# Kernel tuning notes

Measured on AMD Instinct MI355X. Metric: run time of the kernel, lower is better.

Reference implementation:

```python
import jax, jax.numpy as jnp
import numpy as np

B, S, E, H = 1, 4096, 768, 12
DH = E // H  # 64


def setup_inputs() -> dict:
    key = jax.random.key(0)
    ks = jax.random.split(key, 4)
    x = jax.random.normal(ks[0], (B, S, E), dtype=jnp.float32)
    mask = jnp.tril(jnp.ones((S, S), dtype=bool))  # causal mask, broadcast over B,H
    w_qkv = jax.random.normal(ks[1], (3 * E, E), dtype=jnp.float32) * 0.02
    b_qkv = jnp.zeros((3 * E,), dtype=jnp.float32)
    w_out = jax.random.normal(ks[2], (E, E), dtype=jnp.float32) * 0.02
    b_out = jnp.zeros((E,), dtype=jnp.float32)
    return {"x": x, "mask": mask, "w_qkv": w_qkv, "b_qkv": b_qkv,
            "w_out": w_out, "b_out": b_out}


def reference(x, mask, w_qkv, b_qkv, w_out, b_out):
    b, s, e = x.shape
    # qkv projection: torch Linear is x @ W^T + b
    qkv = x @ w_qkv.T + b_qkv                      # [B,S,3E]
    q, k, v = jnp.split(qkv, 3, axis=-1)           # each [B,S,E]
    def heads(t):
        return t.reshape(b, s, H, DH).transpose(0, 2, 1, 3)  # [B,H,S,Dh]
    q, k, v = heads(q), heads(k), heads(v)
    # NOTE: original module does NOT scale by 1/sqrt(head_dim)
    scores = jnp.einsum('bhqd,bhkd->bhqk', q, k)   # [B,H,S,S]
    scores = jnp.where(mask, scores, -jnp.inf)     # masked_fill(mask==0, -inf)
    probs = jax.nn.softmax(scores, axis=-1)        # dropout=0 (eval)
    attn = jnp.einsum('bhqk,bhkd->bhqd', probs, v) # [B,H,S,Dh]
    attn = attn.transpose(0, 2, 1, 3).reshape(b, s, e)
    return attn @ w_out.T + b_out
```

## Files before the change

kernel.cpp:

```cpp
#include <hip/hip_runtime.h>
#include <hip/hip_bf16.h>

#define S_LEN 4096
#define EMB   768
#define NH    12
#define DH    64
#define NCHUNK 4
#define CKL2   10

#define LOG2E 1.44269504088896f

#define NEG_BIG (-1e30f)

#define EXP2F(x) __builtin_amdgcn_exp2f(x)

using bf16x8 = __attribute__((ext_vector_type(8))) short;
using bf16x4 = __attribute__((ext_vector_type(4))) short;
using f32x4  = __attribute__((ext_vector_type(4))) float;

__device__ __forceinline__ short f2bf(float f) {
    __hip_bfloat16 h = __float2bfloat16(f);
    short s; __builtin_memcpy(&s, &h, 2); return s;
}
__device__ __forceinline__ float bf2f(short s) {
    __hip_bfloat16 h; __builtin_memcpy(&h, &s, 2);
    return __bfloat162float(h);
}

__device__ __forceinline__ unsigned cvt_pk_bf16(float a, float b) {
    unsigned r;
    asm("v_cvt_pk_bf16_f32 %0, %1, %2" : "=v"(r) : "v"(a), "v"(b));
    return r;
}

__device__ __forceinline__ void gld_lds16(const void* g, void* l) {
    __builtin_amdgcn_global_load_lds(
        (const __attribute__((address_space(1))) unsigned int*)g,
        (__attribute__((address_space(3))) unsigned int*)l, 16, 0, 0);
}

__device__ __forceinline__ void cvt8(const float* s, short* d, int i) {
    const float4 a = ((const float4*)s)[i * 2];
    const float4 b = ((const float4*)s)[i * 2 + 1];
    bf16x8 o;
    o[0] = f2bf(a.x); o[1] = f2bf(a.y); o[2] = f2bf(a.z); o[3] = f2bf(a.w);
    o[4] = f2bf(b.x); o[5] = f2bf(b.y); o[6] = f2bf(b.z); o[7] = f2bf(b.w);
    ((bf16x8*)d)[i] = o;
}

__global__ __launch_bounds__(256) void cvt_bf16(
    const float* __restrict__ s, short* __restrict__ d, int n8)
{
    const int i = blockIdx.x * 256 + threadIdx.x;
    if (i < n8) cvt8(s, d, i);
}

__global__ __launch_bounds__(256) void cvt3_bf16(
    const float* __restrict__ x,  short* __restrict__ xb,  int n8x,
    const float* __restrict__ wq, short* __restrict__ wqb, int n8q,
    const float* __restrict__ wo, short* __restrict__ wob, int n8o)
{
    int i = blockIdx.x * 256 + threadIdx.x;
    if (i < n8x) { cvt8(x, xb, i); return; }
    i -= n8x;
    if (i < n8q) { cvt8(wq, wqb, i); return; }
    i -= n8q;
    if (i < n8o) cvt8(wo, wob, i);
}

__global__ __launch_bounds__(256) void qkv_gemm(
    const short* __restrict__ Xb, const short* __restrict__ Wb,
    const float* __restrict__ Bias,
    short* __restrict__ Qw, short* __restrict__ Kw, short* __restrict__ Vt)
{
    __shared__ __align__(16) short SMEM[2 * 128 * 64];
    short* As = SMEM;
    short* Bs = SMEM + 128 * 64;

    const int flat = blockIdx.x;
    const int swz = (flat & 7) * 72 + (flat >> 3);
    const int m0 = (swz / 18) * 128;
    const int n0 = (swz % 18) * 128;
    const int t = threadIdx.x;
    const int lane = t & 63, wave = t >> 6;
    const int quad = lane >> 4, l16 = lane & 15;
    const int wm = (wave >> 1) * 64, wn = (wave & 1) * 64;
    const int srow = lane >> 3, scol = (lane & 7) * 8;

    f32x4 acc[4][4] = {};

    for (int k0 = 0; k0 < EMB; k0 += 64) {
        #pragma unroll
        for (int qd = 0; qd < 4; qd++) {
            const int chunk = wave * 4 + qd;
            const int row = chunk * 8 + srow;
            gld_lds16(&Xb[(size_t)(m0 + row) * EMB + k0 + scol], &As[chunk * 512]);
            gld_lds16(&Wb[(size_t)(n0 + row) * EMB + k0 + scol], &Bs[chunk * 512]);
        }
        __syncthreads();

        #pragma unroll
        for (int kb = 0; kb < 2; kb++) {
            bf16x8 af[4], bfr[4];
            #pragma unroll
            for (int i = 0; i < 4; i++)
                af[i] = *(const bf16x8*)&As[(wm + i * 16 + l16) * 64 + kb * 32 + quad * 8];
            #pragma unroll
            for (int j = 0; j < 4; j++)
                bfr[j] = *(const bf16x8*)&Bs[(wn + j * 16 + l16) * 64 + kb * 32 + quad * 8];
            #pragma unroll
            for (int i = 0; i < 4; i++)
                #pragma unroll
                for (int j = 0; j < 4; j++)
                    acc[i][j] = __builtin_amdgcn_mfma_f32_16x16x32_bf16(
                        af[i], bfr[j], acc[i][j], 0, 0, 0);
        }
        __syncthreads();
    }

    const int part = n0 / EMB;

    if (part < 2) {
        const float qs = (part == 0) ? LOG2E : 1.0f;
        short* dst = (part == 0) ? Qw : Kw;
        #pragma unroll
        for (int j = 0; j < 4; j++) {
            const int nl = wn + j * 16 + l16;
            const float bias = Bias[n0 + nl];
            #pragma unroll
            for (int i = 0; i < 4; i++)
                #pragma unroll
                for (int r = 0; r < 4; r++)
                    SMEM[(wm + i * 16 + quad * 4 + r) * 128 + nl] =
                        f2bf((acc[i][j][r] + bias) * qs);
        }
        __syncthreads();
        #pragma unroll
        for (int c = t; c < 2048; c += 256) {
            const int m = c >> 4, noff = (c & 15) * 8;
            const int r768 = (n0 + noff) % EMB;
            const int h = r768 >> 6, d = r768 & 63;
            *(bf16x8*)&dst[((size_t)h * S_LEN + m0 + m) * DH + d] =
                *(const bf16x8*)&SMEM[m * 128 + noff];
        }
    } else {
        #pragma unroll
        for (int j = 0; j < 4; j++) {
            const int nl = wn + j * 16 + l16;
            const float bias = Bias[n0 + nl];
            #pragma unroll
            for (int i = 0; i < 4; i++) {
                short4 v;
                v.x = f2bf(acc[i][j][0] + bias);
                v.y = f2bf(acc[i][j][1] + bias);
                v.z = f2bf(acc[i][j][2] + bias);
                v.w = f2bf(acc[i][j][3] + bias);
                *(short4*)&SMEM[nl * 128 + wm + i * 16 + quad * 4] = v;
            }
        }
        __syncthreads();
        const int vrow0 = n0 - 2 * EMB;
        #pragma unroll
        for (int c = t; c < 2048; c += 256) {
            const int row = c >> 4, off = (c & 15) * 8;
            *(bf16x8*)&Vt[(size_t)(vrow0 + row) * S_LEN + m0 + off] =
                *(const bf16x8*)&SMEM[row * 128 + off];
        }
    }
}

__global__ __launch_bounds__(256, 3) void flash_partial(
    const short* __restrict__ Qw, const short* __restrict__ Kw,
    const short* __restrict__ Vt,
    short* __restrict__ Opart, float* __restrict__ Mpart,
    float* __restrict__ Lpart)
{
    int qt, h, kc;
    {
        const int job = blockIdx.x;
        if (job < 624) {
            h = job / 52;
            const int r = job % 52;
            if (r < 25)      { kc = 0; qt = 7 + r; }
            else if (r < 42) { kc = 1; qt = 15 + (r - 25); }
            else if (r < 51) { kc = 2; qt = 23 + (r - 42); }
            else             { kc = 3; qt = 31; }
        } else {
            const int j2 = job - 624;
            const int w = 7 - j2 / 48;
            const int r = j2 % 48;
            h = r >> 2; kc = r & 3;
            qt = 8 * kc + w - 1;
        }
    }
    const int q0  = qt * 128;
    const int ks0 = kc << CKL2;
    const int KIT = (1 << CKL2) / 128;
    const int nk = min(KIT, (q0 >> 7) - KIT * kc + 1);

    __shared__ __align__(16) short SMEM[128 * 64 + 64 * 128];
    short* Ks = SMEM;
    short* Vs = SMEM + 128 * 64;

    const int t = threadIdx.x;
    const int lane = t & 63, wave = t >> 6;
    const int quad = lane >> 4, l16 = lane & 15;
    const int qw0 = q0 + wave * 32;
    const int swk = (l16 & 7) << 4;
    const int swv = l16 << 4;

    const short* Kh = Kw + (size_t)h * S_LEN * DH;
    const short* Vh = Vt + (size_t)h * DH * S_LEN;

    const int krow = lane >> 3;
    const int kcol = ((lane & 7) ^ krow) << 3;
    const int vrow = lane >> 4;
    const int vsc  = lane & 15;

    bf16x8 qf[2][2];
    #pragma unroll
    for (int i = 0; i < 2; i++)
        #pragma unroll
        for (int kb = 0; kb < 2; kb++)
            qf[i][kb] = *(const bf16x8*)
                &Qw[((size_t)h * S_LEN + qw0 + i * 16 + l16) * DH + kb * 32 + quad * 8];

    bf16x8 vfc;
    {
        const short o1 = (l16 == 0) ? (short)0x3F80 : (short)0;
        #pragma unroll
        for (int c = 0; c < 8; c++) vfc[c] = o1;
    }

    float m_i[2] = {NEG_BIG, NEG_BIG};
    f32x4 o_acc[2][5] = {};

    for (int kt = 0; kt < nk; kt++) {
        const int k0 = ks0 + kt * 128;

        __syncthreads();
        #pragma unroll
        for (int i = 0; i < 4; i++) {
            const int ck = wave * 4 + i;
            const int rk = ck * 8 + krow;
            gld_lds16(&Kh[(size_t)(k0 + rk) * DH + kcol], &Ks[ck * 512]);
            const int rv = ck * 4 + vrow;
            const int vcol = (vsc ^ (rv & 15)) << 3;
            gld_lds16(&Vh[(size_t)rv * S_LEN + k0 + vcol], &Vs[ck * 512]);
        }
        __syncthreads();

        const bool maskn = (k0 + 127 > q0);
        #pragma unroll
        for (int sub = 0; sub < 2; sub++) {
            const int kbase = k0 + sub * 64;
            if (maskn && kbase > qw0 + 31) continue;
            const bool a0 = !(maskn && kbase > qw0 + 15);

            f32x4 sfT[2][4];
            __builtin_amdgcn_s_setprio(1);
            #pragma unroll
            for (int bb = 0; bb < 4; bb++) {
                const int row = (sub * 4 + bb) * 16 + l16;
                bf16x8 kf[2];
                #pragma unroll
                for (int kb = 0; kb < 2; kb++)
                    kf[kb] = *(const bf16x8*)((const char*)Ks
                        + row * 128 + ((kb * 64 + quad * 16) ^ swk));
                sfT[1][bb] = f32x4{};
                #pragma unroll
                for (int kb = 0; kb < 2; kb++)
                    sfT[1][bb] = __builtin_amdgcn_mfma_f32_16x16x32_bf16(
                        kf[kb], qf[1][kb], sfT[1][bb], 0, 0, 0);
                if (a0) {
                    sfT[0][bb] = f32x4{};
                    #pragma unroll
                    for (int kb = 0; kb < 2; kb++)
                        sfT[0][bb] = __builtin_amdgcn_mfma_f32_16x16x32_bf16(
                            kf[kb], qf[0][kb], sfT[0][bb], 0, 0, 0);
                }
            }
            __builtin_amdgcn_s_setprio(0);

            if (maskn) {
                #pragma unroll
                for (int i = 0; i < 2; i++) {
                    if (i == 0 && !a0) continue;
                    const int qg = qw0 + i * 16 + l16;
                    #pragma unroll
                    for (int bb = 0; bb < 4; bb++)
                        #pragma unroll
                        for (int r = 0; r < 4; r++)
                            if (kbase + bb * 16 + quad * 4 + r > qg)
                                sfT[i][bb][r] = NEG_BIG;
                }
            }

            #pragma unroll
            for (int i = 0; i < 2; i++) {
                if (i == 0 && !a0) continue;
                float mx = sfT[i][0][0];
                #pragma unroll
                for (int bb = 0; bb < 4; bb++)
                    #pragma unroll
                    for (int r = 0; r < 4; r++) mx = fmaxf(mx, sfT[i][bb][r]);
                mx = fmaxf(mx, __shfl_xor(mx, 16, 64));
                mx = fmaxf(mx, __shfl_xor(mx, 32, 64));
                if (!__all(mx <= m_i[i] + 8.0f)) {
                    const float mnew = fmaxf(m_i[i], mx);
                    const float alpha = EXP2F(m_i[i] - mnew);
                    m_i[i] = mnew;
                    #pragma unroll
                    for (int db = 0; db < 5; db++) o_acc[i][db] *= alpha;
                }
                #pragma unroll
                for (int bb = 0; bb < 4; bb++)
                    #pragma unroll
                    for (int r = 0; r < 4; r++)
                        sfT[i][bb][r] = EXP2F(sfT[i][bb][r] - m_i[i]);
            }

            __builtin_amdgcn_s_setprio(1);
            #pragma unroll
            for (int bp = 0; bp < 2; bp++) {
                bf16x8 pf[2];
                #pragma unroll
                for (int i = 0; i < 2; i++) {
                    if (i == 0 && !a0) continue;
                    int4 pv;
                    pv.x = (int)cvt_pk_bf16(sfT[i][2 * bp][0],     sfT[i][2 * bp][1]);
                    pv.y = (int)cvt_pk_bf16(sfT[i][2 * bp][2],     sfT[i][2 * bp][3]);
                    pv.z = (int)cvt_pk_bf16(sfT[i][2 * bp + 1][0], sfT[i][2 * bp + 1][1]);
                    pv.w = (int)cvt_pk_bf16(sfT[i][2 * bp + 1][2], sfT[i][2 * bp + 1][3]);
                    pf[i] = __builtin_bit_cast(bf16x8, pv);
                }
                const int colb = (sub * 2 + bp) * 64 + quad * 8;
                #pragma unroll
                for (int db = 0; db < 4; db++) {
                    const char* vb = (const char*)Vs + (db * 16 + l16) * 256;
                    const int2 lo2 = *(const int2*)(vb + (colb ^ swv));
                    const int2 hi2 = *(const int2*)(vb + ((colb + 32) ^ swv));
                    int4 vi; vi.x = lo2.x; vi.y = lo2.y; vi.z = hi2.x; vi.w = hi2.y;
                    const bf16x8 vf = __builtin_bit_cast(bf16x8, vi);
                    o_acc[1][db] = __builtin_amdgcn_mfma_f32_16x16x32_bf16(
                        vf, pf[1], o_acc[1][db], 0, 0, 0);
                    if (a0)
                        o_acc[0][db] = __builtin_amdgcn_mfma_f32_16x16x32_bf16(
                            vf, pf[0], o_acc[0][db], 0, 0, 0);
                }
                o_acc[1][4] = __builtin_amdgcn_mfma_f32_16x16x32_bf16(
                    vfc, pf[1], o_acc[1][4], 0, 0, 0);
                if (a0)
                    o_acc[0][4] = __builtin_amdgcn_mfma_f32_16x16x32_bf16(
                        vfc, pf[0], o_acc[0][4], 0, 0, 0);
            }
            __builtin_amdgcn_s_setprio(0);
        }
    }

    const size_t slab = ((size_t)h * NCHUNK + kc) * S_LEN;

    #pragma unroll
    for (int i = 0; i < 2; i++)
        if (quad == 0) {
            const int q = qw0 + i * 16 + l16;
            Mpart[slab + q] = m_i[i];
            Lpart[slab + q] = o_acc[i][4][0];
        }

    __syncthreads();
    #pragma unroll
    for (int i = 0; i < 2; i++)
        #pragma unroll
        for (int db = 0; db < 4; db++) {
            short4 pk4;
            pk4.x = f2bf(o_acc[i][db][0]); pk4.y = f2bf(o_acc[i][db][1]);
            pk4.z = f2bf(o_acc[i][db][2]); pk4.w = f2bf(o_acc[i][db][3]);
            *(short4*)&SMEM[(wave * 32 + i * 16 + l16) * 72 + db * 16 + quad * 4] = pk4;
        }
    __syncthreads();
    #pragma unroll
    for (int c = t; c < 1024; c += 256) {
        const int row = c >> 3, off = (c & 7) * 8;
        *(bf16x8*)&Opart[(slab + q0 + row) * DH + off] =
            *(const bf16x8*)&SMEM[row * 72 + off];
    }
}

__global__ __launch_bounds__(256) void flash_merge(
    const short* __restrict__ Opart, const float* __restrict__ Mpart,
    const float* __restrict__ Lpart, short* __restrict__ Ctx)
{
    const int row = blockIdx.x * 4 + (threadIdx.x >> 6);
    const int lane = threadIdx.x & 63;
    const int h = row >> 12, q = row & 4095;
    const int nc = (q >> CKL2) + 1;

    float mv[NCHUNK], lv[NCHUNK];
    float M = NEG_BIG;
    #pragma unroll
    for (int c = 0; c < NCHUNK; c++) {
        if (c < nc) {
            mv[c] = Mpart[((size_t)h * NCHUNK + c) * S_LEN + q];
            lv[c] = Lpart[((size_t)h * NCHUNK + c) * S_LEN + q];
            M = fmaxf(M, mv[c]);
        }
    }
    float L = 0.f, O = 0.f;
    #pragma unroll
    for (int c = 0; c < NCHUNK; c++) {
        if (c < nc) {
            const float w = EXP2F(mv[c] - M);
            L += w * lv[c];
            O += w * bf2f(Opart[(((size_t)h * NCHUNK + c) * S_LEN + q) * DH + lane]);
        }
    }
    const float inv = (L > 0.f) ? 1.0f / L : 0.f;
    Ctx[(size_t)q * EMB + h * DH + lane] = f2bf(O * inv);
}

__global__ __launch_bounds__(256) void flash_attn(
    const short* __restrict__ Qw, const short* __restrict__ Kw,
    const short* __restrict__ Vt, short* __restrict__ Ctx)
{
    __shared__ __align__(16) short Ks[128 * 64];
    __shared__ __align__(16) short Vs[64 * 128];
    __shared__ __align__(16) short Ps[4][32 * 128];

    const int h  = blockIdx.y;
    const int qt = (gridDim.x - 1) - blockIdx.x;
    const int q0 = qt * 128;
    const int t = threadIdx.x;
    const int lane = t & 63, wave = t >> 6;
    const int quad = lane >> 4, l16 = lane & 15;
    const int qw0 = q0 + wave * 32;

    bf16x8 qf[2][2];
    #pragma unroll
    for (int i = 0; i < 2; i++)
        #pragma unroll
        for (int kb = 0; kb < 2; kb++)
            qf[i][kb] = *(const bf16x8*)
                &Qw[((size_t)h * S_LEN + qw0 + i * 16 + l16) * DH + kb * 32 + quad * 8];

    float m_i[2][4], l_i[2][4];
    f32x4 o_acc[2][4] = {};
    #pragma unroll
    for (int i = 0; i < 2; i++)
        #pragma unroll
        for (int r = 0; r < 4; r++) { m_i[i][r] = NEG_BIG; l_i[i][r] = 0.f; }

    for (int kt = 0; kt <= qt; kt++) {
        const int k0 = kt * 128;
        __syncthreads();
        for (int c = t; c < 1024; c += 256) {
            const int row = c >> 3, cc = (c & 7) * 8;
            *(bf16x8*)&Ks[row * 64 + cc] =
                *(const bf16x8*)&Kw[((size_t)h * S_LEN + k0 + row) * DH + cc];
        }
        for (int c = t; c < 1024; c += 256) {
            const int row = c >> 4, cc = (c & 15) * 8;
            *(bf16x8*)&Vs[row * 128 + cc] =
                *(const bf16x8*)&Vt[((size_t)h * DH + row) * S_LEN + k0 + cc];
        }
        __syncthreads();

        f32x4 sf[2][8] = {};
        #pragma unroll
        for (int j = 0; j < 8; j++) {
            #pragma unroll
            for (int kb = 0; kb < 2; kb++) {
                const bf16x8 kf = *(const bf16x8*)
                    &Ks[(j * 16 + l16) * 64 + kb * 32 + quad * 8];
                #pragma unroll
                for (int i = 0; i < 2; i++)
                    sf[i][j] = __builtin_amdgcn_mfma_f32_16x16x32_bf16(
                        qf[i][kb], kf, sf[i][j], 0, 0, 0);
            }
        }

        const bool diag = (kt == qt);
        #pragma unroll
        for (int i = 0; i < 2; i++) {
            if (diag) {
                const int qbase = qw0 + i * 16 + quad * 4;
                const int kbase = k0 + l16;
                #pragma unroll
                for (int j = 0; j < 8; j++)
                    #pragma unroll
                    for (int r = 0; r < 4; r++)
                        if (kbase + j * 16 > qbase + r) sf[i][j][r] = NEG_BIG;
            }
            #pragma unroll
            for (int r = 0; r < 4; r++) {
                float mx = sf[i][0][r];
                #pragma unroll
                for (int j = 1; j < 8; j++) mx = fmaxf(mx, sf[i][j][r]);
                #pragma unroll
                for (int off = 1; off < 16; off <<= 1)
                    mx = fmaxf(mx, __shfl_xor(mx, off, 64));
                const float mnew = fmaxf(m_i[i][r], mx);
                const float alpha = EXP2F(m_i[i][r] - mnew);
                m_i[i][r] = mnew;
                float rs = 0.f;
                #pragma unroll
                for (int j = 0; j < 8; j++) {
                    const float p = EXP2F(sf[i][j][r] - mnew);
                    sf[i][j][r] = p;
                    rs += p;
                }
                #pragma unroll
                for (int off = 1; off < 16; off <<= 1)
                    rs += __shfl_xor(rs, off, 64);
                l_i[i][r] = l_i[i][r] * alpha + rs;
                #pragma unroll
                for (int db = 0; db < 4; db++) o_acc[i][db][r] *= alpha;
            }
            #pragma unroll
            for (int j = 0; j < 8; j++)
                #pragma unroll
                for (int r = 0; r < 4; r++)
                    Ps[wave][(i * 16 + quad * 4 + r) * 128 + j * 16 + l16] =
                        f2bf(sf[i][j][r]);
        }

        #pragma unroll
        for (int kb = 0; kb < 4; kb++) {
            bf16x8 pf[2];
            #pragma unroll
            for (int i = 0; i < 2; i++)
                pf[i] = *(const bf16x8*)
                    &Ps[wave][(i * 16 + l16) * 128 + kb * 32 + quad * 8];
            #pragma unroll
            for (int db = 0; db < 4; db++) {
                const bf16x8 vf = *(const bf16x8*)
                    &Vs[(db * 16 + l16) * 128 + kb * 32 + quad * 8];
                #pragma unroll
                for (int i = 0; i < 2; i++)
                    o_acc[i][db] = __builtin_amdgcn_mfma_f32_16x16x32_bf16(
                        pf[i], vf, o_acc[i][db], 0, 0, 0);
            }
        }
    }

    #pragma unroll
    for (int i = 0; i < 2; i++)
        #pragma unroll
        for (int r = 0; r < 4; r++) {
            const float li = l_i[i][r];
            const float inv = (li > 0.f) ? 1.0f / li : 0.f;
            const int m = qw0 + i * 16 + quad * 4 + r;
            #pragma unroll
            for (int db = 0; db < 4; db++) {
                const int d = db * 16 + l16;
                Ctx[(size_t)m * EMB + h * DH + d] = f2bf(o_acc[i][db][r] * inv);
            }
        }
}

__global__ __launch_bounds__(256) void out_gemm(
    const short* __restrict__ A, const short* __restrict__ Wb,
    const float* __restrict__ Bias, float* __restrict__ Out)
{
    __shared__ __align__(16) short As[128 * 64];
    __shared__ __align__(16) short Bs[128 * 64];

    const int flat = blockIdx.x;
    const int swz = (flat & 7) * 24 + (flat >> 3);
    const int m0 = (swz / 6) * 128;
    const int n0 = (swz % 6) * 128;
    const int t = threadIdx.x;
    const int lane = t & 63, wave = t >> 6;
    const int quad = lane >> 4, l16 = lane & 15;
    const int wm = (wave >> 1) * 64, wn = (wave & 1) * 64;
    const int srow = lane >> 3, scol = (lane & 7) * 8;

    f32x4 acc[4][4] = {};

    for (int k0 = 0; k0 < EMB; k0 += 64) {
        #pragma unroll
        for (int qd = 0; qd < 4; qd++) {
            const int chunk = wave * 4 + qd;
            const int row = chunk * 8 + srow;
            gld_lds16(&A [(size_t)(m0 + row) * EMB + k0 + scol], &As[chunk * 512]);
            gld_lds16(&Wb[(size_t)(n0 + row) * EMB + k0 + scol], &Bs[chunk * 512]);
        }
        __syncthreads();

        #pragma unroll
        for (int kb = 0; kb < 2; kb++) {
            bf16x8 af[4], bfr[4];
            #pragma unroll
            for (int i = 0; i < 4; i++)
                af[i] = *(const bf16x8*)&As[(wm + i * 16 + l16) * 64 + kb * 32 + quad * 8];
            #pragma unroll
            for (int j = 0; j < 4; j++)
                bfr[j] = *(const bf16x8*)&Bs[(wn + j * 16 + l16) * 64 + kb * 32 + quad * 8];
            #pragma unroll
            for (int i = 0; i < 4; i++)
                #pragma unroll
                for (int j = 0; j < 4; j++)
                    acc[i][j] = __builtin_amdgcn_mfma_f32_16x16x32_bf16(
                        af[i], bfr[j], acc[i][j], 0, 0, 0);
        }
        __syncthreads();
    }

    #pragma unroll
    for (int j = 0; j < 4; j++) {
        const int n = n0 + wn + j * 16 + l16;
        const float bias = Bias[n];
        #pragma unroll
        for (int i = 0; i < 4; i++)
            #pragma unroll
            for (int r = 0; r < 4; r++) {
                const int m = m0 + wm + i * 16 + quad * 4 + r;
                Out[(size_t)m * EMB + n] = acc[i][j][r] + bias;
            }
    }
}

extern "C" void kernel_launch(void* const* d_in, const int* in_sizes, int n_in,
                              void* d_out, int out_size, void* d_ws, size_t ws_size,
                              hipStream_t stream)
{
    (void)in_sizes; (void)n_in; (void)out_size;
    const float* x     = (const float*)d_in[0];
    const float* w_qkv = (const float*)d_in[2];
    const float* b_qkv = (const float*)d_in[3];
    const float* w_out = (const float*)d_in[4];
    const float* b_out = (const float*)d_in[5];
    float* out = (float*)d_out;

    char* ws = (char*)d_ws;
    const size_t SEG = (size_t)NH * S_LEN * DH * sizeof(short);
    short* Qw  = (short*)(ws);
    short* Kw  = (short*)(ws + SEG);
    short* Vt  = (short*)(ws + 2 * SEG);
    short* Ctx = (short*)(ws + 3 * SEG);
    const size_t OP_OFF = 4 * SEG;
    const size_t OP_SZ  = (size_t)NH * NCHUNK * S_LEN * DH * sizeof(short);
    const size_t ML_SZ  = (size_t)NH * NCHUNK * S_LEN * sizeof(float);
    short* Opart = (short*)(ws + OP_OFF);
    float* Mpart = (float*)(ws + OP_OFF + OP_SZ);
    float* Lpart = (float*)(ws + OP_OFF + OP_SZ + ML_SZ);
    const size_t need = OP_OFF + OP_SZ + 2 * ML_SZ;

    const int XN8 = (S_LEN * EMB) / 8;
    const int WQ8 = (3 * EMB * EMB) / 8;
    const int WO8 = (EMB * EMB) / 8;
    const size_t WO_BYTES = (size_t)EMB * EMB * sizeof(short);
    short* Xb    = (short*)(ws + OP_OFF);
    short* Wqkvb = (short*)(ws + OP_OFF + (size_t)XN8 * 8 * sizeof(short));
    const bool big = ws_size >= need + WO_BYTES;
    short* Woutb = big ? (short*)(ws + need) : (short*)(ws + OP_OFF);

    if (big) {
        const int tot8 = XN8 + WQ8 + WO8;
        cvt3_bf16<<<dim3((tot8 + 255) / 256), 256, 0, stream>>>(
            x, Xb, XN8, w_qkv, Wqkvb, WQ8, w_out, Woutb, WO8);
    } else {
        cvt_bf16<<<dim3((XN8 + 255) / 256), 256, 0, stream>>>(x, Xb, XN8);
        cvt_bf16<<<dim3((WQ8 + 255) / 256), 256, 0, stream>>>(w_qkv, Wqkvb, WQ8);
    }

    qkv_gemm<<<dim3((S_LEN / 128) * ((3 * EMB) / 128)), 256, 0, stream>>>(
        Xb, Wqkvb, b_qkv, Qw, Kw, Vt);

    if (ws_size >= need) {
        flash_partial<<<dim3(960), 256, 0, stream>>>(
            Qw, Kw, Vt, Opart, Mpart, Lpart);
        flash_merge<<<dim3(NH * S_LEN / 4), 256, 0, stream>>>(
            Opart, Mpart, Lpart, Ctx);
    } else {
        flash_attn<<<dim3(S_LEN / 128, NH), 256, 0, stream>>>(Qw, Kw, Vt, Ctx);
    }

    if (!big)
        cvt_bf16<<<dim3((WO8 + 255) / 256), 256, 0, stream>>>(w_out, Woutb, WO8);
    out_gemm<<<dim3((S_LEN / 128) * (EMB / 128)), 256, 0, stream>>>(
        Ctx, Woutb, b_out, out);
}
```

Before: 231.1 us.

## Fuse split-KV flash merge into output projection GEMM A-tile load

Removes the separate flash_merge kernel and the round trip of the Ctx buffer through global memory. The output GEMM now builds each A tile by reading the partial outputs and their max and sum statistics, combining them, normalising, and writing bf16 into shared memory. In exchange, each merge is recomputed by all six N-tile blocks that share a row range. The A-tile load also becomes synchronous register work instead of the direct global-to-LDS loads.

```diff
diff --git a/kernel.cpp b/kernel.cpp
--- a/kernel.cpp
+++ b/kernel.cpp
@@ -558,6 +558,98 @@
         }
 }
 
+__global__ __launch_bounds__(256) void out_gemm_fused(
+    const short* __restrict__ Opart, const float* __restrict__ Mpart,
+    const float* __restrict__ Lpart, const short* __restrict__ Wb,
+    const float* __restrict__ Bias, float* __restrict__ Out)
+{
+    __shared__ __align__(16) short As[128 * 64];
+    __shared__ __align__(16) short Bs[128 * 64];
+
+    const int flat = blockIdx.x;
+    const int swz = (flat & 7) * 24 + (flat >> 3);
+    const int m0 = (swz / 6) * 128;
+    const int n0 = (swz % 6) * 128;
+    const int t = threadIdx.x;
+    const int lane = t & 63, wave = t >> 6;
+    const int quad = lane >> 4, l16 = lane & 15;
+    const int wm = (wave >> 1) * 64, wn = (wave & 1) * 64;
+    const int srow = lane >> 3, scol = (lane & 7) * 8;
+
+    f32x4 acc[4][4] = {};
+
+    for (int k0 = 0; k0 < EMB; k0 += 64) {
+        const int h = k0 >> 6;
+        #pragma unroll
+        for (int qd = 0; qd < 4; qd++) {
+            const int chunk = wave * 4 + qd;
+            const int row = chunk * 8 + srow;
+            gld_lds16(&Wb[(size_t)(n0 + row) * EMB + k0 + scol], &Bs[chunk * 512]);
+
+            const int q = m0 + row;
+            const int nc = (q >> CKL2) + 1;
+            float mv[NCHUNK], lv[NCHUNK];
+            float M = NEG_BIG;
+            #pragma unroll
+            for (int c = 0; c < NCHUNK; c++)
+                if (c < nc) {
+                    mv[c] = Mpart[(((size_t)(h * NCHUNK + c)) << 12) + q];
+                    lv[c] = Lpart[(((size_t)(h * NCHUNK + c)) << 12) + q];
+                    M = fmaxf(M, mv[c]);
+                }
+            float L = 0.f;
+            float o[8] = {};
+            #pragma unroll
+            for (int c = 0; c < NCHUNK; c++)
+                if (c < nc) {
+                    const float w = EXP2F(mv[c] - M);
+                    L += w * lv[c];
+                    const bf16x8 op = *(const bf16x8*)
+                        &Opart[((((size_t)(h * NCHUNK + c)) << 12) + q) * DH + scol];
+                    #pragma unroll
+                    for (int j = 0; j < 8; j++) o[j] += w * bf2f(op[j]);
+                }
+            const float inv = (L > 0.f) ? 1.0f / L : 0.f;
+            bf16x8 a;
+            #pragma unroll
+            for (int j = 0; j < 8; j++) a[j] = f2bf(o[j] * inv);
+            *(bf16x8*)&As[chunk * 512 + lane * 8] = a;
+        }
+        __syncthreads();
+
+        #pragma unroll
+        for (int kb = 0; kb < 2; kb++) {
+            bf16x8 af[4], bfr[4];
+            #pragma unroll
+            for (int i = 0; i < 4; i++)
+                af[i] = *(const bf16x8*)&As[(wm + i * 16 + l16) * 64 + kb * 32 + quad * 8];
+            #pragma unroll
+            for (int j = 0; j < 4; j++)
+                bfr[j] = *(const bf16x8*)&Bs[(wn + j * 16 + l16) * 64 + kb * 32 + quad * 8];
+            #pragma unroll
+            for (int i = 0; i < 4; i++)
+                #pragma unroll
+                for (int j = 0; j < 4; j++)
+                    acc[i][j] = __builtin_amdgcn_mfma_f32_16x16x32_bf16(
+                        af[i], bfr[j], acc[i][j], 0, 0, 0);
+        }
+        __syncthreads();
+    }
+
+    #pragma unroll
+    for (int j = 0; j < 4; j++) {
+        const int n = n0 + wn + j * 16 + l16;
+        const float bias = Bias[n];
+        #pragma unroll
+        for (int i = 0; i < 4; i++)
+            #pragma unroll
+            for (int r = 0; r < 4; r++) {
+                const int m = m0 + wm + i * 16 + quad * 4 + r;
+                Out[(size_t)m * EMB + n] = acc[i][j][r] + bias;
+            }
+    }
+}
+
 __global__ __launch_bounds__(256) void out_gemm(
     const short* __restrict__ A, const short* __restrict__ Wb,
     const float* __restrict__ Bias, float* __restrict__ Out)
@@ -670,14 +762,15 @@
     if (ws_size >= need) {
         flash_partial<<<dim3(960), 256, 0, stream>>>(
             Qw, Kw, Vt, Opart, Mpart, Lpart);
-        flash_merge<<<dim3(NH * S_LEN / 4), 256, 0, stream>>>(
-            Opart, Mpart, Lpart, Ctx);
+        if (!big)
+            cvt_bf16<<<dim3((WO8 + 255) / 256), 256, 0, stream>>>(w_out, Woutb, WO8);
+        out_gemm_fused<<<dim3((S_LEN / 128) * (EMB / 128)), 256, 0, stream>>>(
+            Opart, Mpart, Lpart, Woutb, b_out, out);
     } else {
         flash_attn<<<dim3(S_LEN / 128, NH), 256, 0, stream>>>(Qw, Kw, Vt, Ctx);
-    }
-
-    if (!big)
-        cvt_bf16<<<dim3((WO8 + 255) / 256), 256, 0, stream>>>(w_out, Woutb, WO8);
-    out_gemm<<<dim3((S_LEN / 128) * (EMB / 128)), 256, 0, stream>>>(
-        Ctx, Woutb, b_out, out);
-}
+        if (!big)
+            cvt_bf16<<<dim3((WO8 + 255) / 256), 256, 0, stream>>>(w_out, Woutb, WO8);
+        out_gemm<<<dim3((S_LEN / 128) * (EMB / 128)), 256, 0, stream>>>(
+            Ctx, Woutb, b_out, out);
+    }
+}
```

Result: slower. 310.0 us (+34.2%).
